# Kernel optimization log

Measured on AMD Instinct MI355X. Metric: run time of the kernel, lower is better.

## Reference

```python
import jax, jax.numpy as jnp
import numpy as np

N = 100000          # nodes
E = 3200000         # edges (avg degree 32)
K = 3               # TAGConv hops
ALPHA = 1.0 / 9.0   # top-k fraction
EPS = 1e-5          # InstanceNorm eps


def setup_inputs() -> dict:
    key = jax.random.key(0)
    ks = jax.random.split(key, 9)
    x = jax.random.uniform(ks[0], (N,), dtype=jnp.float32)
    edge_index = jax.random.randint(ks[1], (2, E), 0, N, dtype=jnp.int64)
    edge_attr = jax.random.normal(ks[2], (E,), dtype=jnp.float32)
    # TAGConv weights: K+1 hop matrices per layer (PyG uses bias once per layer)
    W1 = jax.random.normal(ks[3], (K + 1, 1, 8), dtype=jnp.float32) * 0.5
    b1 = jax.random.normal(ks[4], (8,), dtype=jnp.float32) * 0.1
    W2 = jax.random.normal(ks[5], (K + 1, 8, 8), dtype=jnp.float32) * 0.2
    b2 = jax.random.normal(ks[6], (8,), dtype=jnp.float32) * 0.1
    W3 = jax.random.normal(ks[7], (K + 1, 8, 1), dtype=jnp.float32) * 0.2
    b3 = jax.random.normal(ks[8], (1,), dtype=jnp.float32) * 0.1
    k = int(N * ALPHA)  # 11111
    return {"x": x, "edge_attr": edge_attr, "W1": W1, "b1": b1,
            "W2": W2, "b2": b2, "W3": W3, "b3": b3,
            "edge_index": edge_index, "k": k}


def _tagconv(h, src, dst, norm, W, b):
    # out = sum_{i=0..K} (A_norm^i h) @ W[i] + b
    out = h @ W[0]
    for i in range(1, W.shape[0]):
        h = jax.ops.segment_sum(norm[:, None] * h[src], dst, num_segments=N)
        out = out + h @ W[i]
    return out + b


def reference(x, edge_attr, W1, b1, W2, b2, W3, b3, edge_index, k):
    src, dst = edge_index[0], edge_index[1]
    w = jnp.abs(edge_attr)
    # gcn_norm without self-loops (PyG TAGConv default)
    deg = jax.ops.segment_sum(w, dst, num_segments=N)
    deg_safe = jnp.where(deg > 0, deg, 1.0)
    dinv = jnp.where(deg > 0, jax.lax.rsqrt(deg_safe), 0.0)
    norm = dinv[src] * w * dinv[dst]

    h = x[:, None]  # [N, 1]
    h = jax.nn.relu(_tagconv(h, src, dst, norm, W1, b1))
    h = jax.nn.relu(_tagconv(h, src, dst, norm, W2, b2))
    h = jax.nn.relu(_tagconv(h, src, dst, norm, W3, b3))

    # InstanceNorm(1): normalize over nodes per channel (biased var, no affine)
    mu = jnp.mean(h, axis=0)
    var = jnp.mean((h - mu) ** 2, axis=0)
    h = ((h - mu) * jax.lax.rsqrt(var + EPS))[:, 0]  # [N]

    # diff_top_k
    order = jnp.argsort(-h)
    topk = order[:k]
    top_k_vec = jnp.full((N,), -1.0, dtype=h.dtype).at[topk].set(1.0)
    k_smallest = jnp.abs(h[topk[k - 1]])
    soft = jax.nn.sigmoid(h - k_smallest + top_k_vec * 0.1)

    return jnp.stack([h, soft], axis=1)  # [N, 2]
```

## Files before the change

### kernel.cpp

```cpp
#include <hip/hip_runtime.h>
#include <math.h>

#define NN 100000
#define NE 3200000
#define NBKT 782
#define NBLK 196
#define EPB 16384
#define BCAP 6144
#define HTPB 1024

static constexpr int TPB = 256;
static constexpr int GRID_N = (NN + TPB - 1) / TPB;
static constexpr int GRID_N4 = (NN * 4 + TPB - 1) / TPB;

__global__ void k_init(const int* __restrict__ kptr, unsigned* __restrict__ prefix,
                       int* __restrict__ target, double* __restrict__ stats) {
  *prefix = 0u;
  *target = *kptr;
  stats[0] = 0.0;
  stats[1] = 0.0;
}

__global__ void b_hist(const int* __restrict__ dst, int* __restrict__ histT) {
  __shared__ int h[NBKT];
  for (int i = threadIdx.x; i < NBKT; i += HTPB) h[i] = 0;
  __syncthreads();
  int base = blockIdx.x * EPB;
  #pragma unroll 4
  for (int i = 0; i < EPB / HTPB; ++i) {
    int e = base + i * HTPB + threadIdx.x;
    if (e < NE) atomicAdd(&h[dst[e] >> 7], 1);
  }
  __syncthreads();
  for (int i = threadIdx.x; i < NBKT; i += HTPB)
    histT[i * NBLK + blockIdx.x] = h[i];
}

__global__ void b_rowscan(int* __restrict__ histT, int* __restrict__ rowsum) {
  int r = blockIdx.x, lane = threadIdx.x;
  int base = r * NBLK;
  int v[4]; int s = 0;
  #pragma unroll
  for (int i = 0; i < 4; ++i) {
    int c = lane * 4 + i;
    v[i] = (c < NBLK) ? histT[base + c] : 0;
    s += v[i];
  }
  int pre = s;
  for (int off = 1; off < 64; off <<= 1) {
    int t = __shfl_up(pre, off);
    if (lane >= off) pre += t;
  }
  int excl = pre - s;
  #pragma unroll
  for (int i = 0; i < 4; ++i) {
    int c = lane * 4 + i;
    if (c < NBLK) histT[base + c] = excl;
    excl += v[i];
  }
  if (lane == 63) rowsum[r] = pre;
}

__global__ void b_base(const int* __restrict__ rowsum, int* __restrict__ bucketBase,
                       int* __restrict__ rowptr) {
  if (threadIdx.x == 0) {
    int acc = 0;
    for (int b = 0; b < NBKT; ++b) { bucketBase[b] = acc; acc += rowsum[b]; }
    bucketBase[NBKT] = NE;
    rowptr[NN] = NE;
  }
}

__global__ void b_scatter(const int* __restrict__ src, const int* __restrict__ dst,
                          const float* __restrict__ ea, const int* __restrict__ histT,
                          const int* __restrict__ bucketBase, int2* __restrict__ grouped) {
  __shared__ int cursor[NBKT];
  for (int b = threadIdx.x; b < NBKT; b += HTPB)
    cursor[b] = bucketBase[b] + histT[b * NBLK + blockIdx.x];
  __syncthreads();
  int base = blockIdx.x * EPB;
  #pragma unroll 4
  for (int i = 0; i < EPB / HTPB; ++i) {
    int e = base + i * HTPB + threadIdx.x;
    if (e < NE) {
      int d = dst[e];
      int pos = atomicAdd(&cursor[d >> 7], 1);
      int meta = ((d & 127) << 17) | src[e];
      grouped[pos] = make_int2(meta, __float_as_int(fabsf(ea[e])));
    }
  }
}

__global__ void __launch_bounds__(512) b_sortdeg(const int* __restrict__ bucketBase,
                                                 const int2* __restrict__ grouped,
                                                 int2* __restrict__ ed, int* __restrict__ rowptr,
                                                 float* __restrict__ dinv) {
  __shared__ int hist[128];
  __shared__ float degf[128];
  __shared__ int binoff[128];
  __shared__ int cursor[128];
  __shared__ int2 out[BCAP];
  int b = blockIdx.x, t = threadIdx.x;
  int base = bucketBase[b], n = bucketBase[b + 1] - base;
  if (t < 128) { hist[t] = 0; degf[t] = 0.0f; }
  __syncthreads();
  for (int j = t; j < n; j += 512) {
    int2 el = grouped[base + j];
    int dl = el.x >> 17;
    atomicAdd(&hist[dl], 1);
    atomicAdd(&degf[dl], __int_as_float(el.y));
  }
  __syncthreads();
  if (t == 0) {
    int acc = 0;
    for (int i = 0; i < 128; ++i) { binoff[i] = acc; acc += hist[i]; }
  }
  __syncthreads();
  if (t < 128) {
    cursor[t] = binoff[t];
    int node = b * 128 + t;
    if (node < NN) {
      rowptr[node] = base + binoff[t];
      float dg = degf[t];
      dinv[node] = (dg > 0.0f) ? (1.0f / sqrtf(dg)) : 0.0f;
    }
  }
  __syncthreads();
  for (int j = t; j < n; j += 512) {
    int2 el = grouped[base + j];
    int dl = el.x >> 17;
    int pos = atomicAdd(&cursor[dl], 1);
    if (pos < BCAP) out[pos] = el;
  }
  __syncthreads();
  for (int j = t; j < n; j += 512) {
    int2 el = out[j];
    ed[base + j] = make_int2(el.x & 0x1FFFF, el.y);
  }
}

__global__ void g_prop1fix(const int* __restrict__ rowptr, int2* __restrict__ ed,
                           const float* __restrict__ dinv, const float* __restrict__ hin,
                           float* __restrict__ hout) {
  int t = blockIdx.x * TPB + threadIdx.x;
  int n = t >> 2, r = t & 3;
  if (n >= NN) return;
  int s0 = rowptr[n], s1 = rowptr[n + 1];
  float dn = dinv[n];
  float acc = 0.0f;
  for (int i = s0 + r; i < s1; i += 4) {
    int2 e = ed[i];
    float w = __int_as_float(e.y) * dinv[e.x] * dn;
    ed[i].y = __float_as_int(w);
    acc += w * hin[e.x];
  }
  acc += __shfl_xor(acc, 1);
  acc += __shfl_xor(acc, 2);
  if (r == 0) hout[n] = acc;
}

__global__ void g_prop1(const int* __restrict__ rowptr, const int2* __restrict__ ed,
                        const float* __restrict__ hin, float* __restrict__ hout) {
  int t = blockIdx.x * TPB + threadIdx.x;
  int n = t >> 2, r = t & 3;
  if (n >= NN) return;
  int s0 = rowptr[n], s1 = rowptr[n + 1];
  float acc = 0.0f;
  for (int i = s0 + r; i < s1; i += 4) {
    int2 e = ed[i];
    acc += __int_as_float(e.y) * hin[e.x];
  }
  acc += __shfl_xor(acc, 1);
  acc += __shfl_xor(acc, 2);
  if (r == 0) hout[n] = acc;
}

__global__ void g_prop1add(const int* __restrict__ rowptr, const int2* __restrict__ ed,
                           const float* __restrict__ gsrc, const float* __restrict__ addv,
                           float* __restrict__ out) {
  int t = blockIdx.x * TPB + threadIdx.x;
  int n = t >> 2, r = t & 3;
  if (n >= NN) return;
  int s0 = rowptr[n], s1 = rowptr[n + 1];
  float acc = 0.0f;
  for (int i = s0 + r; i < s1; i += 4) {
    int2 e = ed[i];
    acc += __int_as_float(e.y) * gsrc[e.x];
  }
  acc += __shfl_xor(acc, 1);
  acc += __shfl_xor(acc, 2);
  if (r == 0) out[n] = addv[n] + acc;
}

__global__ void g_prop1addS(const int* __restrict__ rowptr, const int2* __restrict__ ed,
                            const float* __restrict__ gsrc, const float* __restrict__ addv,
                            float* __restrict__ out, double* __restrict__ stats) {
  int t = blockIdx.x * TPB + threadIdx.x;
  int n = t >> 2, r = t & 3;
  float contrib = 0.0f;
  if (n < NN) {
    int s0 = rowptr[n], s1 = rowptr[n + 1];
    float acc = 0.0f;
    for (int i = s0 + r; i < s1; i += 4) {
      int2 e = ed[i];
      acc += __int_as_float(e.y) * gsrc[e.x];
    }
    acc += __shfl_xor(acc, 1);
    acc += __shfl_xor(acc, 2);
    if (r == 0) {
      float v = fmaxf(addv[n] + acc, 0.0f);
      out[n] = v;
      contrib = v;
    }
  }
  double s = (double)contrib, s2 = (double)contrib * (double)contrib;
  #pragma unroll
  for (int o = 32; o > 0; o >>= 1) {
    s  += __shfl_down(s, o);
    s2 += __shfl_down(s2, o);
  }
  __shared__ double ls[4], ls2[4];
  int lane = threadIdx.x & 63, w = threadIdx.x >> 6;
  if (lane == 0) { ls[w] = s; ls2[w] = s2; }
  __syncthreads();
  if (threadIdx.x == 0) {
    atomicAdd(&stats[0], ls[0] + ls[1] + ls[2] + ls[3]);
    atomicAdd(&stats[1], ls2[0] + ls2[1] + ls2[2] + ls2[3]);
  }
}

__global__ void g_prop1c(const int* __restrict__ rowptr, const int2* __restrict__ ed,
                         const float* __restrict__ x, const float* __restrict__ p1,
                         const float* __restrict__ p2, const float* __restrict__ hin,
                         const float* __restrict__ W, const float* __restrict__ b,
                         float* __restrict__ out) {
  int t = blockIdx.x * TPB + threadIdx.x;
  int n = t >> 2, r = t & 3;
  if (n >= NN) return;
  int s0 = rowptr[n], s1 = rowptr[n + 1];
  float acc = 0.0f;
  for (int i = s0 + r; i < s1; i += 4) {
    int2 e = ed[i];
    acc += __int_as_float(e.y) * hin[e.x];
  }
  acc += __shfl_xor(acc, 1);
  acc += __shfl_xor(acc, 2);
  if (r == 0) {
    float h0 = x[n], h1 = p1[n], h2 = p2[n], h3 = acc;
    float* op = out + (size_t)n * 8;
    #pragma unroll
    for (int j = 0; j < 8; ++j) {
      float v = b[j] + h0 * W[j] + h1 * W[8 + j] + h2 * W[16 + j] + h3 * W[24 + j];
      op[j] = fmaxf(v, 0.0f);
    }
  }
}

__global__ void g_prop8(const int* __restrict__ rowptr, const int2* __restrict__ ed,
                        const float* __restrict__ hin, float* __restrict__ hout) {
  int t = blockIdx.x * TPB + threadIdx.x;
  int n = t >> 2, r = t & 3;
  if (n >= NN) return;
  int s0 = rowptr[n], s1 = rowptr[n + 1];
  float a0 = 0, a1 = 0, a2 = 0, a3 = 0, a4 = 0, a5 = 0, a6 = 0, a7 = 0;
  for (int i = s0 + r; i < s1; i += 4) {
    int2 e = ed[i];
    float w = __int_as_float(e.y);
    const float4* hp = (const float4*)(hin + (size_t)e.x * 8);
    float4 xx = hp[0], yy = hp[1];
    a0 += w * xx.x; a1 += w * xx.y; a2 += w * xx.z; a3 += w * xx.w;
    a4 += w * yy.x; a5 += w * yy.y; a6 += w * yy.z; a7 += w * yy.w;
  }
  #pragma unroll
  for (int m = 1; m <= 2; m <<= 1) {
    a0 += __shfl_xor(a0, m); a1 += __shfl_xor(a1, m);
    a2 += __shfl_xor(a2, m); a3 += __shfl_xor(a3, m);
    a4 += __shfl_xor(a4, m); a5 += __shfl_xor(a5, m);
    a6 += __shfl_xor(a6, m); a7 += __shfl_xor(a7, m);
  }
  if (r == 0) {
    float4* op = (float4*)(hout + (size_t)n * 8);
    op[0] = make_float4(a0, a1, a2, a3);
    op[1] = make_float4(a4, a5, a6, a7);
  }
}

__global__ void g_prop8l3(const int* __restrict__ rowptr, const int2* __restrict__ ed,
                          const float* __restrict__ p0, const float* __restrict__ p1,
                          const float* __restrict__ hin,
                          const float* __restrict__ W2, const float* __restrict__ b2,
                          const float* __restrict__ W3, const float* __restrict__ b3,
                          float* __restrict__ g0o, float* __restrict__ s1o,
                          float* __restrict__ s2o, float* __restrict__ s3o) {
  int t = blockIdx.x * TPB + threadIdx.x;
  int n = t >> 2, r = t & 3;
  if (n >= NN) return;
  int s0 = rowptr[n], s1 = rowptr[n + 1];
  float a0 = 0, a1 = 0, a2 = 0, a3 = 0, a4 = 0, a5 = 0, a6 = 0, a7 = 0;
  for (int i = s0 + r; i < s1; i += 4) {
    int2 e = ed[i];
    float w = __int_as_float(e.y);
    const float4* hp = (const float4*)(hin + (size_t)e.x * 8);
    float4 xx = hp[0], yy = hp[1];
    a0 += w * xx.x; a1 += w * xx.y; a2 += w * xx.z; a3 += w * xx.w;
    a4 += w * yy.x; a5 += w * yy.y; a6 += w * yy.z; a7 += w * yy.w;
  }
  #pragma unroll
  for (int m = 1; m <= 2; m <<= 1) {
    a0 += __shfl_xor(a0, m); a1 += __shfl_xor(a1, m);
    a2 += __shfl_xor(a2, m); a3 += __shfl_xor(a3, m);
    a4 += __shfl_xor(a4, m); a5 += __shfl_xor(a5, m);
    a6 += __shfl_xor(a6, m); a7 += __shfl_xor(a7, m);
  }
  if (r == 0) {
    float h[4][8];
    const float4* hp = (const float4*)(p0 + (size_t)n * 8);
    float4 u = hp[0], v4 = hp[1];
    h[0][0]=u.x; h[0][1]=u.y; h[0][2]=u.z; h[0][3]=u.w; h[0][4]=v4.x; h[0][5]=v4.y; h[0][6]=v4.z; h[0][7]=v4.w;
    hp = (const float4*)(p1 + (size_t)n * 8);
    u = hp[0]; v4 = hp[1];
    h[1][0]=u.x; h[1][1]=u.y; h[1][2]=u.z; h[1][3]=u.w; h[1][4]=v4.x; h[1][5]=v4.y; h[1][6]=v4.z; h[1][7]=v4.w;
    hp = (const float4*)(hin + (size_t)n * 8);
    u = hp[0]; v4 = hp[1];
    h[2][0]=u.x; h[2][1]=u.y; h[2][2]=u.z; h[2][3]=u.w; h[2][4]=v4.x; h[2][5]=v4.y; h[2][6]=v4.z; h[2][7]=v4.w;
    h[3][0]=a0; h[3][1]=a1; h[3][2]=a2; h[3][3]=a3; h[3][4]=a4; h[3][5]=a5; h[3][6]=a6; h[3][7]=a7;
    float hv[8];
    #pragma unroll
    for (int j = 0; j < 8; ++j) {
      float v = b2[j];
      #pragma unroll
      for (int i = 0; i < 4; ++i) {
        #pragma unroll
        for (int f = 0; f < 8; ++f) v += h[i][f] * W2[i * 64 + f * 8 + j];
      }
      hv[j] = fmaxf(v, 0.0f);
    }
    float g0 = b3[0], sv1 = 0, sv2 = 0, sv3 = 0;
    #pragma unroll
    for (int f = 0; f < 8; ++f) {
      g0  += hv[f] * W3[f];
      sv1 += hv[f] * W3[8 + f];
      sv2 += hv[f] * W3[16 + f];
      sv3 += hv[f] * W3[24 + f];
    }
    g0o[n] = g0; s1o[n] = sv1; s2o[n] = sv2; s3o[n] = sv3;
  }
}

__global__ void k_normkey(const float* __restrict__ h, const double* __restrict__ stats,
                          float* __restrict__ hn, unsigned* __restrict__ key) {
  int n = blockIdx.x * TPB + threadIdx.x;
  if (n >= NN) return;
  double mu = stats[0] / (double)NN;
  double var = stats[1] / (double)NN - mu * mu;
  if (var < 0.0) var = 0.0;
  double invs = 1.0 / sqrt(var + 1e-5);
  float v = (float)(((double)h[n] - mu) * invs);
  hn[n] = v;
  unsigned u = __float_as_uint(v);
  unsigned asc = (u & 0x80000000u) ? ~u : (u | 0x80000000u);
  key[n] = ~asc;
}

template <int SHIFT, unsigned MASK>
__global__ void k_hist(const unsigned* __restrict__ key, const unsigned* __restrict__ prefix,
                       unsigned* __restrict__ hist) {
  __shared__ unsigned lh[256];
  lh[threadIdx.x] = 0;
  __syncthreads();
  int n = blockIdx.x * TPB + threadIdx.x;
  unsigned pfx = *prefix;
  if (n < NN) {
    unsigned kk = key[n];
    if ((kk & MASK) == pfx) atomicAdd(&lh[(kk >> SHIFT) & 0xffu], 1u);
  }
  __syncthreads();
  if (lh[threadIdx.x]) atomicAdd(&hist[threadIdx.x], lh[threadIdx.x]);
}

template <int SHIFT>
__global__ void k_pick(const unsigned* __restrict__ hist, unsigned* __restrict__ prefix,
                       int* __restrict__ target) {
  int t = *target;
  unsigned cum = 0;
  for (int b = 0; b < 256; ++b) {
    unsigned c = hist[b];
    if ((int)(cum + c) >= t) {
      *prefix |= ((unsigned)b) << SHIFT;
      *target = t - (int)cum;
      return;
    }
    cum += c;
  }
}

__global__ void k_count(const unsigned* __restrict__ key, const unsigned* __restrict__ prefix,
                        int* __restrict__ partials) {
  int n = blockIdx.x * TPB + threadIdx.x;
  unsigned T = *prefix;
  bool eq = (n < NN) && (key[n] == T);
  unsigned long long meq = __ballot(eq);
  __shared__ int ce[4];
  int lane = threadIdx.x & 63, w = threadIdx.x >> 6;
  if (lane == 0) ce[w] = __popcll(meq);
  __syncthreads();
  if (threadIdx.x == 0) partials[blockIdx.x] = ce[0] + ce[1] + ce[2] + ce[3];
}

__global__ void k_scan(const int* __restrict__ partials, int* __restrict__ offs) {
  if (threadIdx.x == 0) {
    int acc = 0;
    for (int b = 0; b < GRID_N; ++b) { offs[b] = acc; acc += partials[b]; }
  }
}

__global__ void k_final(const float* __restrict__ hn, const unsigned* __restrict__ key,
                        const unsigned* __restrict__ prefix, const int* __restrict__ offs,
                        const int* __restrict__ rptr, float* __restrict__ out) {
  int n = blockIdx.x * TPB + threadIdx.x;
  unsigned T = *prefix;
  int r = *rptr;
  bool eq = false, lt = false;
  float v = 0.0f;
  if (n < NN) {
    unsigned kk = key[n];
    eq = (kk == T);
    lt = (kk < T);
    v = hn[n];
  }
  unsigned long long m = __ballot(eq);
  __shared__ int wc[4];
  int lane = threadIdx.x & 63, w = threadIdx.x >> 6;
  if (lane == 0) wc[w] = __popcll(m);
  __syncthreads();
  int off = offs[blockIdx.x];
  for (int i = 0; i < w; ++i) off += wc[i];
  off += __popcll(m & ((1ull << lane) - 1ull));
  if (n >= NN) return;
  bool top = lt || (eq && off < r);
  unsigned asc = ~T;
  unsigned orig = (asc & 0x80000000u) ? (asc & 0x7fffffffu) : ~asc;
  float thr = fabsf(__uint_as_float(orig));
  float tkv = top ? 1.0f : -1.0f;
  float z = v - thr + tkv * 0.1f;
  out[2 * n]     = v;
  out[2 * n + 1] = 1.0f / (1.0f + expf(-z));
}

extern "C" void kernel_launch(void* const* d_in, const int* in_sizes, int n_in,
                              void* d_out, int out_size, void* d_ws, size_t ws_size,
                              hipStream_t stream) {
  const float* x       = (const float*)d_in[0];
  const float* ea      = (const float*)d_in[1];
  const float* W1      = (const float*)d_in[2];
  const float* b1      = (const float*)d_in[3];
  const float* W2      = (const float*)d_in[4];
  const float* b2      = (const float*)d_in[5];
  const float* W3      = (const float*)d_in[6];
  const float* b3      = (const float*)d_in[7];
  const int* ei        = (const int*)d_in[8];
  const int* kptr      = (const int*)d_in[9];
  float* out           = (float*)d_out;

  const int* src = ei;
  const int* dst = ei + NE;

  char* ws = (char*)d_ws;
  size_t off = 0;
  auto alloc = [&](size_t bytes) -> void* {
    void* p = ws + off;
    off += (bytes + 255) & ~(size_t)255;
    return p;
  };

  int2*     ed       = (int2*)alloc((size_t)NE * 8);
  int2*     grouped  = (int2*)alloc((size_t)NE * 8);
  int*      histT    = (int*)alloc((size_t)NBKT * NBLK * 4);
  int*      rowsum   = (int*)alloc((size_t)NBKT * 4);
  int*      bucketBase = (int*)alloc(((size_t)NBKT + 1) * 4);
  int*      rowptr   = (int*)alloc(((size_t)NN + 1) * 4);
  float*    dinv     = (float*)alloc((size_t)NN * 4);
  float*    pA       = (float*)alloc((size_t)NN * 8 * 4);
  float*    pB       = (float*)alloc((size_t)NN * 8 * 4);
  float*    h1       = (float*)alloc((size_t)NN * 8 * 4);
  float*    g0       = (float*)alloc((size_t)NN * 4);
  float*    s1       = (float*)alloc((size_t)NN * 4);
  float*    s2       = (float*)alloc((size_t)NN * 4);
  float*    s3       = (float*)alloc((size_t)NN * 4);
  float*    u        = (float*)alloc((size_t)NN * 4);
  float*    v        = (float*)alloc((size_t)NN * 4);
  float*    h3       = (float*)alloc((size_t)NN * 4);
  float*    hn       = (float*)alloc((size_t)NN * 4);
  unsigned* key      = (unsigned*)alloc((size_t)NN * 4);
  double*   stats    = (double*)alloc(2 * 8);
  unsigned* hist4    = (unsigned*)alloc(4 * 256 * 4);
  int*      partials = (int*)alloc(512 * 4);
  int*      offs     = (int*)alloc(512 * 4);
  unsigned* prefix   = (unsigned*)alloc(4);
  int*      target   = (int*)alloc(4);

  k_init<<<1, 1, 0, stream>>>(kptr, prefix, target, stats);

  b_hist<<<NBLK, HTPB, 0, stream>>>(dst, histT);
  b_rowscan<<<NBKT, 64, 0, stream>>>(histT, rowsum);
  b_base<<<1, 64, 0, stream>>>(rowsum, bucketBase, rowptr);
  b_scatter<<<NBLK, HTPB, 0, stream>>>(src, dst, ea, histT, bucketBase, grouped);
  b_sortdeg<<<NBKT, 512, 0, stream>>>(bucketBase, grouped, ed, rowptr, dinv);

  g_prop1fix<<<GRID_N4, TPB, 0, stream>>>(rowptr, ed, dinv, x, pA);
  g_prop1<<<GRID_N4, TPB, 0, stream>>>(rowptr, ed, pA, pB);
  g_prop1c<<<GRID_N4, TPB, 0, stream>>>(rowptr, ed, x, pA, pB, pB, W1, b1, h1);

  g_prop8<<<GRID_N4, TPB, 0, stream>>>(rowptr, ed, h1, pA);
  g_prop8<<<GRID_N4, TPB, 0, stream>>>(rowptr, ed, pA, pB);
  g_prop8l3<<<GRID_N4, TPB, 0, stream>>>(rowptr, ed, h1, pA, pB, W2, b2, W3, b3,
                                         g0, s1, s2, s3);

  g_prop1add<<<GRID_N4, TPB, 0, stream>>>(rowptr, ed, s3, s2, u);
  g_prop1add<<<GRID_N4, TPB, 0, stream>>>(rowptr, ed, u, s1, v);
  g_prop1addS<<<GRID_N4, TPB, 0, stream>>>(rowptr, ed, v, g0, h3, stats);

  k_normkey<<<GRID_N, TPB, 0, stream>>>(h3, stats, hn, key);

  hipMemsetAsync(hist4, 0, 4096, stream);
  k_hist<24, 0x00000000u><<<GRID_N, TPB, 0, stream>>>(key, prefix, hist4);
  k_pick<24><<<1, 1, 0, stream>>>(hist4, prefix, target);
  k_hist<16, 0xFF000000u><<<GRID_N, TPB, 0, stream>>>(key, prefix, hist4 + 256);
  k_pick<16><<<1, 1, 0, stream>>>(hist4 + 256, prefix, target);
  k_hist<8, 0xFFFF0000u><<<GRID_N, TPB, 0, stream>>>(key, prefix, hist4 + 512);
  k_pick<8><<<1, 1, 0, stream>>>(hist4 + 512, prefix, target);
  k_hist<0, 0xFFFFFF00u><<<GRID_N, TPB, 0, stream>>>(key, prefix, hist4 + 768);
  k_pick<0><<<1, 1, 0, stream>>>(hist4 + 768, prefix, target);

  k_count<<<GRID_N, TPB, 0, stream>>>(key, prefix, partials);
  k_scan<<<1, 64, 0, stream>>>(partials, offs);
  k_final<<<GRID_N, TPB, 0, stream>>>(hn, key, prefix, offs, target, out);
}
```

Baseline: 575.2 us.

## Fuse all TAGConv propagations into a cooperative kernel with LDS-resident edge slices

Replaces the nine separate per-hop propagation kernels with one cooperative persistent kernel that uses grid.sync between hops. Each of the 512 blocks owns a node range balanced by edge count (found by binary search on rowptr) and caches its normalized edge slice in shared memory, so later hops read edges from LDS instead of global memory. x and dinv are packed into one float2 array to save a gather in the first pass. The trade-offs are grid-wide barriers, a requirement that all blocks are co-resident, and no bounds check if a slice exceeds the LDS capacity.

```diff
diff --git a/kernel.cpp b/kernel.cpp
--- a/kernel.cpp
+++ b/kernel.cpp
@@ -1,5 +1,8 @@
 #include <hip/hip_runtime.h>
+#include <hip/hip_cooperative_groups.h>
 #include <math.h>
+
+namespace cg = cooperative_groups;
 
 #define NN 100000
 #define NE 3200000
@@ -8,10 +11,12 @@
 #define EPB 16384
 #define BCAP 6144
 #define HTPB 1024
+#define NMB 512
+#define MTPB 512
+#define SLICE_CAP 8064
 
 static constexpr int TPB = 256;
 static constexpr int GRID_N = (NN + TPB - 1) / TPB;
-static constexpr int GRID_N4 = (NN * 4 + TPB - 1) / TPB;
 
 __global__ void k_init(const int* __restrict__ kptr, unsigned* __restrict__ prefix,
                        int* __restrict__ target, double* __restrict__ stats) {
@@ -93,8 +98,9 @@
 
 __global__ void __launch_bounds__(512) b_sortdeg(const int* __restrict__ bucketBase,
                                                  const int2* __restrict__ grouped,
+                                                 const float* __restrict__ x,
                                                  int2* __restrict__ ed, int* __restrict__ rowptr,
-                                                 float* __restrict__ dinv) {
+                                                 float2* __restrict__ xd) {
   __shared__ int hist[128];
   __shared__ float degf[128];
   __shared__ int binoff[128];
@@ -122,7 +128,8 @@
     if (node < NN) {
       rowptr[node] = base + binoff[t];
       float dg = degf[t];
-      dinv[node] = (dg > 0.0f) ? (1.0f / sqrtf(dg)) : 0.0f;
+      float dv = (dg > 0.0f) ? (1.0f / sqrtf(dg)) : 0.0f;
+      xd[node] = make_float2(x[node], dv);
     }
   }
   __syncthreads();
@@ -139,211 +146,201 @@
   }
 }
 
-__global__ void g_prop1fix(const int* __restrict__ rowptr, int2* __restrict__ ed,
-                           const float* __restrict__ dinv, const float* __restrict__ hin,
-                           float* __restrict__ hout) {
-  int t = blockIdx.x * TPB + threadIdx.x;
-  int n = t >> 2, r = t & 3;
-  if (n >= NN) return;
-  int s0 = rowptr[n], s1 = rowptr[n + 1];
-  float dn = dinv[n];
-  float acc = 0.0f;
-  for (int i = s0 + r; i < s1; i += 4) {
-    int2 e = ed[i];
-    float w = __int_as_float(e.y) * dinv[e.x] * dn;
-    ed[i].y = __float_as_int(w);
-    acc += w * hin[e.x];
-  }
-  acc += __shfl_xor(acc, 1);
-  acc += __shfl_xor(acc, 2);
-  if (r == 0) hout[n] = acc;
-}
-
-__global__ void g_prop1(const int* __restrict__ rowptr, const int2* __restrict__ ed,
-                        const float* __restrict__ hin, float* __restrict__ hout) {
-  int t = blockIdx.x * TPB + threadIdx.x;
-  int n = t >> 2, r = t & 3;
-  if (n >= NN) return;
-  int s0 = rowptr[n], s1 = rowptr[n + 1];
-  float acc = 0.0f;
-  for (int i = s0 + r; i < s1; i += 4) {
-    int2 e = ed[i];
-    acc += __int_as_float(e.y) * hin[e.x];
-  }
-  acc += __shfl_xor(acc, 1);
-  acc += __shfl_xor(acc, 2);
-  if (r == 0) hout[n] = acc;
-}
-
-__global__ void g_prop1add(const int* __restrict__ rowptr, const int2* __restrict__ ed,
-                           const float* __restrict__ gsrc, const float* __restrict__ addv,
-                           float* __restrict__ out) {
-  int t = blockIdx.x * TPB + threadIdx.x;
-  int n = t >> 2, r = t & 3;
-  if (n >= NN) return;
-  int s0 = rowptr[n], s1 = rowptr[n + 1];
-  float acc = 0.0f;
-  for (int i = s0 + r; i < s1; i += 4) {
-    int2 e = ed[i];
-    acc += __int_as_float(e.y) * gsrc[e.x];
-  }
-  acc += __shfl_xor(acc, 1);
-  acc += __shfl_xor(acc, 2);
-  if (r == 0) out[n] = addv[n] + acc;
-}
-
-__global__ void g_prop1addS(const int* __restrict__ rowptr, const int2* __restrict__ ed,
-                            const float* __restrict__ gsrc, const float* __restrict__ addv,
-                            float* __restrict__ out, double* __restrict__ stats) {
-  int t = blockIdx.x * TPB + threadIdx.x;
-  int n = t >> 2, r = t & 3;
-  float contrib = 0.0f;
-  if (n < NN) {
-    int s0 = rowptr[n], s1 = rowptr[n + 1];
-    float acc = 0.0f;
-    for (int i = s0 + r; i < s1; i += 4) {
-      int2 e = ed[i];
-      acc += __int_as_float(e.y) * gsrc[e.x];
+__global__ void e_ranges(const int* __restrict__ rowptr, int* __restrict__ nb) {
+  int b = threadIdx.x + blockIdx.x * 1024;
+  if (b > NMB) return;
+  if (b == 0) { nb[0] = 0; return; }
+  if (b == NMB) { nb[NMB] = NN; return; }
+  int targ = (int)(((long long)NE * b) / NMB);
+  int lo = 0, hi = NN;
+  while (lo < hi) {
+    int mid = (lo + hi) >> 1;
+    if (rowptr[mid] < targ) lo = mid + 1; else hi = mid;
+  }
+  nb[b] = lo;
+}
+
+#define SPROP(GSRC, STORE)                                          \
+  for (int m = nlo + g; m < nhi; m += 128) {                        \
+    int s0 = rowptr[m], s1e = rowptr[m + 1];                        \
+    float acc = 0.f;                                                \
+    for (int i = s0 + r; i < s1e; i += 4) {                         \
+      int2 e = slice[i - ebase];                                    \
+      acc += __int_as_float(e.y) * GSRC[e.x];                       \
+    }                                                               \
+    acc += __shfl_xor(acc, 1);                                      \
+    acc += __shfl_xor(acc, 2);                                      \
+    if (r == 0) { STORE; }                                          \
+  }
+
+#define PROP8_HEAD(HSRC)                                            \
+  for (int m = nlo + g; m < nhi; m += 128) {                        \
+    int s0 = rowptr[m], s1e = rowptr[m + 1];                        \
+    float a0=0,a1=0,a2=0,a3=0,a4=0,a5=0,a6=0,a7=0;                  \
+    for (int i = s0 + r; i < s1e; i += 4) {                         \
+      int2 e = slice[i - ebase];                                    \
+      float w = __int_as_float(e.y);                                \
+      const float4* hp = (const float4*)(HSRC + (size_t)e.x * 8);   \
+      float4 xx = hp[0], yy = hp[1];                                \
+      a0 += w*xx.x; a1 += w*xx.y; a2 += w*xx.z; a3 += w*xx.w;       \
+      a4 += w*yy.x; a5 += w*yy.y; a6 += w*yy.z; a7 += w*yy.w;       \
+    }                                                               \
+    a0+=__shfl_xor(a0,1); a1+=__shfl_xor(a1,1); a2+=__shfl_xor(a2,1); a3+=__shfl_xor(a3,1); \
+    a4+=__shfl_xor(a4,1); a5+=__shfl_xor(a5,1); a6+=__shfl_xor(a6,1); a7+=__shfl_xor(a7,1); \
+    a0+=__shfl_xor(a0,2); a1+=__shfl_xor(a1,2); a2+=__shfl_xor(a2,2); a3+=__shfl_xor(a3,2); \
+    a4+=__shfl_xor(a4,2); a5+=__shfl_xor(a5,2); a6+=__shfl_xor(a6,2); a7+=__shfl_xor(a7,2);
+
+__global__ void __launch_bounds__(MTPB) mega(
+    const int* __restrict__ rowptr, const int2* __restrict__ edg,
+    const float2* __restrict__ xd, const int* __restrict__ nb,
+    const float* __restrict__ W1, const float* __restrict__ b1,
+    const float* __restrict__ W2, const float* __restrict__ b2,
+    const float* __restrict__ W3, const float* __restrict__ b3,
+    float* __restrict__ pA, float* __restrict__ pB,
+    float* __restrict__ uu, float* __restrict__ vv,
+    float* __restrict__ pA8, float* __restrict__ pB8, float* __restrict__ h1,
+    float* __restrict__ g0, float* __restrict__ s1o, float* __restrict__ s2o,
+    float* __restrict__ s3o, float* __restrict__ h3, double* __restrict__ stats) {
+  __shared__ int2 slice[SLICE_CAP];
+  __shared__ double ls[8], ls2[8];
+  cg::grid_group grid = cg::this_grid();
+  const int tid = threadIdx.x;
+  const int r = tid & 3, g = tid >> 2;
+  const int nlo = nb[blockIdx.x], nhi = nb[blockIdx.x + 1];
+  const int ebase = rowptr[nlo];
+
+  for (int m = nlo + g; m < nhi; m += 128) {
+    float2 xm = xd[m];
+    int s0 = rowptr[m], s1e = rowptr[m + 1];
+    float acc = 0.f;
+    for (int i = s0 + r; i < s1e; i += 4) {
+      int2 e = edg[i];
+      float2 v = xd[e.x];
+      float w = __int_as_float(e.y) * v.y * xm.y;
+      slice[i - ebase] = make_int2(e.x, __float_as_int(w));
+      acc += w * v.x;
+    }
+    acc += __shfl_xor(acc, 1);
+    acc += __shfl_xor(acc, 2);
+    if (r == 0) pA[m] = acc;
+  }
+  __syncthreads();
+  grid.sync();
+
+  SPROP(pA, pB[m] = acc)
+  grid.sync();
+
+  for (int m = nlo + g; m < nhi; m += 128) {
+    int s0 = rowptr[m], s1e = rowptr[m + 1];
+    float acc = 0.f;
+    for (int i = s0 + r; i < s1e; i += 4) {
+      int2 e = slice[i - ebase];
+      acc += __int_as_float(e.y) * pB[e.x];
     }
     acc += __shfl_xor(acc, 1);
     acc += __shfl_xor(acc, 2);
     if (r == 0) {
-      float v = fmaxf(addv[n] + acc, 0.0f);
-      out[n] = v;
-      contrib = v;
-    }
-  }
-  double s = (double)contrib, s2 = (double)contrib * (double)contrib;
+      float h0 = xd[m].x, p1v = pA[m], p2v = pB[m], p3v = acc;
+      float* op = h1 + (size_t)m * 8;
+      #pragma unroll
+      for (int j = 0; j < 8; ++j)
+        op[j] = fmaxf(b1[j] + h0 * W1[j] + p1v * W1[8 + j] + p2v * W1[16 + j] + p3v * W1[24 + j], 0.f);
+    }
+  }
+  grid.sync();
+
+  PROP8_HEAD(h1)
+    if (r == 0) {
+      float* op = pA8 + (size_t)m * 8;
+      *(float4*)op = make_float4(a0, a1, a2, a3);
+      *(float4*)(op + 4) = make_float4(a4, a5, a6, a7);
+    }
+  }
+  grid.sync();
+
+  PROP8_HEAD(pA8)
+    if (r == 0) {
+      float* op = pB8 + (size_t)m * 8;
+      *(float4*)op = make_float4(a0, a1, a2, a3);
+      *(float4*)(op + 4) = make_float4(a4, a5, a6, a7);
+    }
+  }
+  grid.sync();
+
+  PROP8_HEAD(pB8)
+    if (r == 0) {
+      float h[4][8];
+      const float4* hp = (const float4*)(h1 + (size_t)m * 8);
+      float4 u = hp[0], v4 = hp[1];
+      h[0][0]=u.x; h[0][1]=u.y; h[0][2]=u.z; h[0][3]=u.w; h[0][4]=v4.x; h[0][5]=v4.y; h[0][6]=v4.z; h[0][7]=v4.w;
+      hp = (const float4*)(pA8 + (size_t)m * 8);
+      u = hp[0]; v4 = hp[1];
+      h[1][0]=u.x; h[1][1]=u.y; h[1][2]=u.z; h[1][3]=u.w; h[1][4]=v4.x; h[1][5]=v4.y; h[1][6]=v4.z; h[1][7]=v4.w;
+      hp = (const float4*)(pB8 + (size_t)m * 8);
+      u = hp[0]; v4 = hp[1];
+      h[2][0]=u.x; h[2][1]=u.y; h[2][2]=u.z; h[2][3]=u.w; h[2][4]=v4.x; h[2][5]=v4.y; h[2][6]=v4.z; h[2][7]=v4.w;
+      h[3][0]=a0; h[3][1]=a1; h[3][2]=a2; h[3][3]=a3; h[3][4]=a4; h[3][5]=a5; h[3][6]=a6; h[3][7]=a7;
+      float hv[8];
+      #pragma unroll
+      for (int j = 0; j < 8; ++j) {
+        float v = b2[j];
+        #pragma unroll
+        for (int i2 = 0; i2 < 4; ++i2) {
+          #pragma unroll
+          for (int f = 0; f < 8; ++f) v += h[i2][f] * W2[i2 * 64 + f * 8 + j];
+        }
+        hv[j] = fmaxf(v, 0.0f);
+      }
+      float g0v = b3[0], sv1 = 0, sv2 = 0, sv3 = 0;
+      #pragma unroll
+      for (int f = 0; f < 8; ++f) {
+        g0v += hv[f] * W3[f];
+        sv1 += hv[f] * W3[8 + f];
+        sv2 += hv[f] * W3[16 + f];
+        sv3 += hv[f] * W3[24 + f];
+      }
+      g0[m] = g0v; s1o[m] = sv1; s2o[m] = sv2; s3o[m] = sv3;
+    }
+  }
+  grid.sync();
+
+  SPROP(s3o, uu[m] = s2o[m] + acc)
+  grid.sync();
+
+  SPROP(uu, vv[m] = s1o[m] + acc)
+  grid.sync();
+
+  double cs = 0.0, cs2 = 0.0;
+  for (int m = nlo + g; m < nhi; m += 128) {
+    int s0 = rowptr[m], s1e = rowptr[m + 1];
+    float acc = 0.f;
+    for (int i = s0 + r; i < s1e; i += 4) {
+      int2 e = slice[i - ebase];
+      acc += __int_as_float(e.y) * vv[e.x];
+    }
+    acc += __shfl_xor(acc, 1);
+    acc += __shfl_xor(acc, 2);
+    if (r == 0) {
+      float hv3 = fmaxf(g0[m] + acc, 0.0f);
+      h3[m] = hv3;
+      cs += (double)hv3;
+      cs2 += (double)hv3 * (double)hv3;
+    }
+  }
   #pragma unroll
   for (int o = 32; o > 0; o >>= 1) {
-    s  += __shfl_down(s, o);
-    s2 += __shfl_down(s2, o);
-  }
-  __shared__ double ls[4], ls2[4];
-  int lane = threadIdx.x & 63, w = threadIdx.x >> 6;
-  if (lane == 0) { ls[w] = s; ls2[w] = s2; }
-  __syncthreads();
-  if (threadIdx.x == 0) {
-    atomicAdd(&stats[0], ls[0] + ls[1] + ls[2] + ls[3]);
-    atomicAdd(&stats[1], ls2[0] + ls2[1] + ls2[2] + ls2[3]);
-  }
-}
-
-__global__ void g_prop1c(const int* __restrict__ rowptr, const int2* __restrict__ ed,
-                         const float* __restrict__ x, const float* __restrict__ p1,
-                         const float* __restrict__ p2, const float* __restrict__ hin,
-                         const float* __restrict__ W, const float* __restrict__ b,
-                         float* __restrict__ out) {
-  int t = blockIdx.x * TPB + threadIdx.x;
-  int n = t >> 2, r = t & 3;
-  if (n >= NN) return;
-  int s0 = rowptr[n], s1 = rowptr[n + 1];
-  float acc = 0.0f;
-  for (int i = s0 + r; i < s1; i += 4) {
-    int2 e = ed[i];
-    acc += __int_as_float(e.y) * hin[e.x];
-  }
-  acc += __shfl_xor(acc, 1);
-  acc += __shfl_xor(acc, 2);
-  if (r == 0) {
-    float h0 = x[n], h1 = p1[n], h2 = p2[n], h3 = acc;
-    float* op = out + (size_t)n * 8;
+    cs  += __shfl_down(cs, o);
+    cs2 += __shfl_down(cs2, o);
+  }
+  int lane = tid & 63, w = tid >> 6;
+  if (lane == 0) { ls[w] = cs; ls2[w] = cs2; }
+  __syncthreads();
+  if (tid == 0) {
+    double a = 0, b = 0;
     #pragma unroll
-    for (int j = 0; j < 8; ++j) {
-      float v = b[j] + h0 * W[j] + h1 * W[8 + j] + h2 * W[16 + j] + h3 * W[24 + j];
-      op[j] = fmaxf(v, 0.0f);
-    }
-  }
-}
-
-__global__ void g_prop8(const int* __restrict__ rowptr, const int2* __restrict__ ed,
-                        const float* __restrict__ hin, float* __restrict__ hout) {
-  int t = blockIdx.x * TPB + threadIdx.x;
-  int n = t >> 2, r = t & 3;
-  if (n >= NN) return;
-  int s0 = rowptr[n], s1 = rowptr[n + 1];
-  float a0 = 0, a1 = 0, a2 = 0, a3 = 0, a4 = 0, a5 = 0, a6 = 0, a7 = 0;
-  for (int i = s0 + r; i < s1; i += 4) {
-    int2 e = ed[i];
-    float w = __int_as_float(e.y);
-    const float4* hp = (const float4*)(hin + (size_t)e.x * 8);
-    float4 xx = hp[0], yy = hp[1];
-    a0 += w * xx.x; a1 += w * xx.y; a2 += w * xx.z; a3 += w * xx.w;
-    a4 += w * yy.x; a5 += w * yy.y; a6 += w * yy.z; a7 += w * yy.w;
-  }
-  #pragma unroll
-  for (int m = 1; m <= 2; m <<= 1) {
-    a0 += __shfl_xor(a0, m); a1 += __shfl_xor(a1, m);
-    a2 += __shfl_xor(a2, m); a3 += __shfl_xor(a3, m);
-    a4 += __shfl_xor(a4, m); a5 += __shfl_xor(a5, m);
-    a6 += __shfl_xor(a6, m); a7 += __shfl_xor(a7, m);
-  }
-  if (r == 0) {
-    float4* op = (float4*)(hout + (size_t)n * 8);
-    op[0] = make_float4(a0, a1, a2, a3);
-    op[1] = make_float4(a4, a5, a6, a7);
-  }
-}
-
-__global__ void g_prop8l3(const int* __restrict__ rowptr, const int2* __restrict__ ed,
-                          const float* __restrict__ p0, const float* __restrict__ p1,
-                          const float* __restrict__ hin,
-                          const float* __restrict__ W2, const float* __restrict__ b2,
-                          const float* __restrict__ W3, const float* __restrict__ b3,
-                          float* __restrict__ g0o, float* __restrict__ s1o,
-                          float* __restrict__ s2o, float* __restrict__ s3o) {
-  int t = blockIdx.x * TPB + threadIdx.x;
-  int n = t >> 2, r = t & 3;
-  if (n >= NN) return;
-  int s0 = rowptr[n], s1 = rowptr[n + 1];
-  float a0 = 0, a1 = 0, a2 = 0, a3 = 0, a4 = 0, a5 = 0, a6 = 0, a7 = 0;
-  for (int i = s0 + r; i < s1; i += 4) {
-    int2 e = ed[i];
-    float w = __int_as_float(e.y);
-    const float4* hp = (const float4*)(hin + (size_t)e.x * 8);
-    float4 xx = hp[0], yy = hp[1];
-    a0 += w * xx.x; a1 += w * xx.y; a2 += w * xx.z; a3 += w * xx.w;
-    a4 += w * yy.x; a5 += w * yy.y; a6 += w * yy.z; a7 += w * yy.w;
-  }
-  #pragma unroll
-  for (int m = 1; m <= 2; m <<= 1) {
-    a0 += __shfl_xor(a0, m); a1 += __shfl_xor(a1, m);
-    a2 += __shfl_xor(a2, m); a3 += __shfl_xor(a3, m);
-    a4 += __shfl_xor(a4, m); a5 += __shfl_xor(a5, m);
-    a6 += __shfl_xor(a6, m); a7 += __shfl_xor(a7, m);
-  }
-  if (r == 0) {
-    float h[4][8];
-    const float4* hp = (const float4*)(p0 + (size_t)n * 8);
-    float4 u = hp[0], v4 = hp[1];
-    h[0][0]=u.x; h[0][1]=u.y; h[0][2]=u.z; h[0][3]=u.w; h[0][4]=v4.x; h[0][5]=v4.y; h[0][6]=v4.z; h[0][7]=v4.w;
-    hp = (const float4*)(p1 + (size_t)n * 8);
-    u = hp[0]; v4 = hp[1];
-    h[1][0]=u.x; h[1][1]=u.y; h[1][2]=u.z; h[1][3]=u.w; h[1][4]=v4.x; h[1][5]=v4.y; h[1][6]=v4.z; h[1][7]=v4.w;
-    hp = (const float4*)(hin + (size_t)n * 8);
-    u = hp[0]; v4 = hp[1];
-    h[2][0]=u.x; h[2][1]=u.y; h[2][2]=u.z; h[2][3]=u.w; h[2][4]=v4.x; h[2][5]=v4.y; h[2][6]=v4.z; h[2][7]=v4.w;
-    h[3][0]=a0; h[3][1]=a1; h[3][2]=a2; h[3][3]=a3; h[3][4]=a4; h[3][5]=a5; h[3][6]=a6; h[3][7]=a7;
-    float hv[8];
-    #pragma unroll
-    for (int j = 0; j < 8; ++j) {
-      float v = b2[j];
-      #pragma unroll
-      for (int i = 0; i < 4; ++i) {
-        #pragma unroll
-        for (int f = 0; f < 8; ++f) v += h[i][f] * W2[i * 64 + f * 8 + j];
-      }
-      hv[j] = fmaxf(v, 0.0f);
-    }
-    float g0 = b3[0], sv1 = 0, sv2 = 0, sv3 = 0;
-    #pragma unroll
-    for (int f = 0; f < 8; ++f) {
-      g0  += hv[f] * W3[f];
-      sv1 += hv[f] * W3[8 + f];
-      sv2 += hv[f] * W3[16 + f];
-      sv3 += hv[f] * W3[24 + f];
-    }
-    g0o[n] = g0; s1o[n] = sv1; s2o[n] = sv2; s3o[n] = sv3;
+    for (int i = 0; i < 8; ++i) { a += ls[i]; b += ls2[i]; }
+    atomicAdd(&stats[0], a);
+    atomicAdd(&stats[1], b);
   }
 }
 
@@ -479,16 +476,19 @@
   int*      rowsum   = (int*)alloc((size_t)NBKT * 4);
   int*      bucketBase = (int*)alloc(((size_t)NBKT + 1) * 4);
   int*      rowptr   = (int*)alloc(((size_t)NN + 1) * 4);
-  float*    dinv     = (float*)alloc((size_t)NN * 4);
-  float*    pA       = (float*)alloc((size_t)NN * 8 * 4);
-  float*    pB       = (float*)alloc((size_t)NN * 8 * 4);
+  float2*   xd       = (float2*)alloc((size_t)NN * 8);
+  int*      nbp      = (int*)alloc(((size_t)NMB + 1) * 4);
+  float*    pA       = (float*)alloc((size_t)NN * 4);
+  float*    pB       = (float*)alloc((size_t)NN * 4);
+  float*    uu       = (float*)alloc((size_t)NN * 4);
+  float*    vv       = (float*)alloc((size_t)NN * 4);
+  float*    pA8      = (float*)alloc((size_t)NN * 8 * 4);
+  float*    pB8      = (float*)alloc((size_t)NN * 8 * 4);
   float*    h1       = (float*)alloc((size_t)NN * 8 * 4);
   float*    g0       = (float*)alloc((size_t)NN * 4);
   float*    s1       = (float*)alloc((size_t)NN * 4);
   float*    s2       = (float*)alloc((size_t)NN * 4);
   float*    s3       = (float*)alloc((size_t)NN * 4);
-  float*    u        = (float*)alloc((size_t)NN * 4);
-  float*    v        = (float*)alloc((size_t)NN * 4);
   float*    h3       = (float*)alloc((size_t)NN * 4);
   float*    hn       = (float*)alloc((size_t)NN * 4);
   unsigned* key      = (unsigned*)alloc((size_t)NN * 4);
@@ -505,20 +505,24 @@
   b_rowscan<<<NBKT, 64, 0, stream>>>(histT, rowsum);
   b_base<<<1, 64, 0, stream>>>(rowsum, bucketBase, rowptr);
   b_scatter<<<NBLK, HTPB, 0, stream>>>(src, dst, ea, histT, bucketBase, grouped);
-  b_sortdeg<<<NBKT, 512, 0, stream>>>(bucketBase, grouped, ed, rowptr, dinv);
-
-  g_prop1fix<<<GRID_N4, TPB, 0, stream>>>(rowptr, ed, dinv, x, pA);
-  g_prop1<<<GRID_N4, TPB, 0, stream>>>(rowptr, ed, pA, pB);
-  g_prop1c<<<GRID_N4, TPB, 0, stream>>>(rowptr, ed, x, pA, pB, pB, W1, b1, h1);
-
-  g_prop8<<<GRID_N4, TPB, 0, stream>>>(rowptr, ed, h1, pA);
-  g_prop8<<<GRID_N4, TPB, 0, stream>>>(rowptr, ed, pA, pB);
-  g_prop8l3<<<GRID_N4, TPB, 0, stream>>>(rowptr, ed, h1, pA, pB, W2, b2, W3, b3,
-                                         g0, s1, s2, s3);
-
-  g_prop1add<<<GRID_N4, TPB, 0, stream>>>(rowptr, ed, s3, s2, u);
-  g_prop1add<<<GRID_N4, TPB, 0, stream>>>(rowptr, ed, u, s1, v);
-  g_prop1addS<<<GRID_N4, TPB, 0, stream>>>(rowptr, ed, v, g0, h3, stats);
+  b_sortdeg<<<NBKT, 512, 0, stream>>>(bucketBase, grouped, x, ed, rowptr, xd);
+  e_ranges<<<1, 1024, 0, stream>>>(rowptr, nbp);
+
+  {
+    const int* rp = rowptr;
+    const int2* edp = ed;
+    const float2* xdp = xd;
+    const int* nbq = nbp;
+    void* margs[] = {
+      (void*)&rp, (void*)&edp, (void*)&xdp, (void*)&nbq,
+      (void*)&W1, (void*)&b1, (void*)&W2, (void*)&b2, (void*)&W3, (void*)&b3,
+      (void*)&pA, (void*)&pB, (void*)&uu, (void*)&vv,
+      (void*)&pA8, (void*)&pB8, (void*)&h1,
+      (void*)&g0, (void*)&s1, (void*)&s2, (void*)&s3,
+      (void*)&h3, (void*)&stats
+    };
+    hipLaunchCooperativeKernel((void*)mega, dim3(NMB), dim3(MTPB), margs, 0, stream);
+  }
 
   k_normkey<<<GRID_N, TPB, 0, stream>>>(h3, stats, hn, key);
 
```

After: 960.1 us. 66.9% more time.
